# Performance work log

Measured on AMD Instinct MI355X. Metric: run time of the kernel, lower is better.

Reference implementation:

```python
import jax, jax.numpy as jnp
import numpy as np

EPS = 1e-6
H = 16       # query heads
KVH = 8      # kv heads
DH = 64      # head dim
HID = 1024


def _rms_norm(x, w, eps=EPS):
    ms = jnp.mean(jnp.square(x.astype(jnp.float32)), axis=-1, keepdims=True) + eps
    y = x.astype(jnp.float32) * jax.lax.rsqrt(ms)
    if w is not None:
        y = y * w.astype(jnp.float32)
    return y.astype(x.dtype)


def _rotate_half(x):
    h = x.shape[-1] // 2
    return jnp.concatenate([-x[..., h:], x[..., :h]], axis=-1)


def _multi_axis_rope(x, cos, sin, ndim):
    # x: [B,S,Hd,DH]; cos/sin: [S, rot_total]
    dh = x.shape[-1]
    rot = 2 * (dh // (2 * ndim))
    outs = []
    for i in range(ndim):
        sl = slice(i * rot, (i + 1) * rot)
        xp = x[..., sl]
        cp = cos[:, sl][:, None, :]   # [S,1,rot] broadcasts over heads
        sp = sin[:, sl][:, None, :]
        outs.append(xp * cp + _rotate_half(xp) * sp)
    return jnp.concatenate(outs, axis=-1)


def setup_inputs() -> dict:
    key = jax.random.key(0)
    ks = jax.random.split(key, 10)
    B, S = 4, 2048
    inp = {
        "hidden_states": jax.random.normal(ks[0], (B, S, HID), dtype=jnp.float32),
        "cos": jax.random.uniform(ks[1], (S, DH), dtype=jnp.float32, minval=-1.0, maxval=1.0),
        "sin": jax.random.uniform(ks[2], (S, DH), dtype=jnp.float32, minval=-1.0, maxval=1.0),
        "position_ids": jax.random.randint(ks[3], (B, S, 2), 0, 64).astype(jnp.int64),
        "attention_mask": jnp.ones((B, S), dtype=bool),
        "Wq": jax.random.normal(ks[4], (HID, H * DH), dtype=jnp.float32) * 0.02,
        "Wk": jax.random.normal(ks[5], (HID, KVH * DH), dtype=jnp.float32) * 0.02,
        "Wv": jax.random.normal(ks[6], (HID, KVH * DH), dtype=jnp.float32) * 0.02,
        "Wo": jax.random.normal(ks[7], (H * DH, HID), dtype=jnp.float32) * 0.02,
        "q_norm_w": jnp.ones((DH,), dtype=jnp.float32),
        "k_norm_w": jnp.ones((DH,), dtype=jnp.float32),
    }
    return inp


def reference(hidden_states, cos, sin, position_ids, attention_mask, Wq, Wk, Wv, Wo, q_norm_w, k_norm_w):
    B, S, _ = hidden_states.shape
    ndim = int(position_ids.shape[-1])

    q = (hidden_states @ Wq).reshape(B, S, H, DH)
    k = (hidden_states @ Wk).reshape(B, S, KVH, DH)
    v = (hidden_states @ Wv).reshape(B, S, KVH, DH)

    q = _rms_norm(q, q_norm_w)
    k = _rms_norm(k, k_norm_w)
    v = _rms_norm(v, None)  # v_norm has no scale

    q = _multi_axis_rope(q, cos, sin, ndim)
    k = _multi_axis_rope(k, cos, sin, ndim)

    # [B, heads, S, DH]; repeat kv heads for GQA
    q = q.transpose(0, 2, 1, 3)
    k = jnp.repeat(k.transpose(0, 2, 1, 3), H // KVH, axis=1)
    v = jnp.repeat(v.transpose(0, 2, 1, 3), H // KVH, axis=1)

    scores = jnp.einsum("bhqd,bhkd->bhqk", q, k)  # scaling = 1.0
    key_mask = attention_mask[:, None, None, :]
    scores = jnp.where(key_mask, scores, jnp.finfo(scores.dtype).min)
    probs = jax.nn.softmax(scores.astype(jnp.float32), axis=-1).astype(v.dtype)

    out = jnp.einsum("bhqk,bhkd->bhqd", probs, v)
    out = out.transpose(0, 2, 1, 3).reshape(B, S, H * DH)
    out = jnp.where(attention_mask[:, :, None], out, 0.0)
    return out @ Wo
```

## Files before the change

kernel.cpp:

```cpp
#include <hip/hip_runtime.h>
#include <stdint.h>
#include <stddef.h>

typedef unsigned short u16;
typedef unsigned int   u32;
typedef unsigned short u16x8 __attribute__((ext_vector_type(8)));
typedef unsigned int   u32x2 __attribute__((ext_vector_type(2)));
typedef __attribute__((ext_vector_type(8))) __bf16 bf16x8;
typedef __attribute__((ext_vector_type(4))) float f32x4;

__device__ __forceinline__ float bf2f(u16 v){
  union { unsigned u; float f; } x; x.u = ((unsigned)v) << 16; return x.f;
}
__device__ __forceinline__ u16 f2bf(float f){
  union { float f; unsigned u; } x; x.f = f;
  return (u16)((x.u + 0x7fffu + ((x.u >> 16) & 1u)) >> 16);
}

__device__ __forceinline__ float exp2_fast(float x){
  float r; asm("v_exp_f32 %0, %1" : "=v"(r) : "v"(x)); return r;
}
__device__ __forceinline__ u32 cvt_pk_bf16(float lo, float hi){
  u32 r; asm("v_cvt_pk_bf16_f32 %0, %1, %2" : "=v"(r) : "v"(lo), "v"(hi)); return r;
}

__device__ __forceinline__ f32x4 mfma16(bf16x8 a, bf16x8 b, f32x4 c){
  return __builtin_amdgcn_mfma_f32_16x16x32_bf16(a, b, c, 0, 0, 0);
}

#define AS1 __attribute__((address_space(1)))
#define AS3 __attribute__((address_space(3)))
__device__ __forceinline__ void gload_lds16(const void* g, void* l){
  __builtin_amdgcn_global_load_lds((const AS1 void*)g, (AS3 void*)l, 16, 0, 0);
}

__global__ void f32_to_bf16_swz(const float* __restrict__ in, u16* __restrict__ out,
                                int total_chunks){
  for (int i = blockIdx.x * blockDim.x + threadIdx.x; i < total_chunks;
       i += gridDim.x * blockDim.x){
    int row = i >> 7, c = i & 127;
    int cs = (c & ~7) | ((c & 7) ^ (row & 7));
    const float* p = in + ((size_t)i << 3);
    float4 v0 = *(const float4*)p;
    float4 v1 = *(const float4*)(p + 4);
    u16x8 o = { f2bf(v0.x), f2bf(v0.y), f2bf(v0.z), f2bf(v0.w),
                f2bf(v1.x), f2bf(v1.y), f2bf(v1.z), f2bf(v1.w) };
    *(u16x8*)(out + (((size_t)row << 7) + cs) * 8) = o;
  }
}

__global__ void conv_transpose_swz(const float* __restrict__ in, u16* __restrict__ out,
                                   int R, int C){
  __shared__ float t[32][33];
  int c0 = blockIdx.x * 32, r0 = blockIdx.y * 32;
  int tx = threadIdx.x, ty = threadIdx.y;
  t[ty][tx] = in[(size_t)(r0 + ty) * C + c0 + tx];
  __syncthreads();
  int tid = ty * 32 + tx;
  if (tid < 128){
    int orow = tid >> 2, oc = tid & 3;
    int gr = c0 + orow;
    int gc = (r0 >> 3) + oc;
    int gcs = (gc & ~7) | ((gc & 7) ^ (gr & 7));
    u16x8 v;
#pragma unroll
    for (int i = 0; i < 8; i++) v[i] = f2bf(t[oc * 8 + i][orow]);
    *(u16x8*)(out + (size_t)gr * R + gcs * 8) = v;
  }
}

__global__ void pack_cs(const float* __restrict__ cosb, const float* __restrict__ sinb,
                        float2* __restrict__ cs, int n){
  int i = blockIdx.x * 256 + threadIdx.x;
  if (i < n) cs[i] = (float2){cosb[i], sinb[i]};
}

template<int BM, int WM, int EPI>
__global__ __launch_bounds__(512, 2)
void gemm256(const u16* __restrict__ A, const u16* __restrict__ Bt,
             void* __restrict__ Cv, int M, int N, int K,
             const float2* __restrict__ cs, const float* __restrict__ qw,
             const float* __restrict__ kw, u16* __restrict__ Qn,
             u16* __restrict__ Kn, u16* __restrict__ Vn){
  constexpr int MF = WM / 16;
  constexpr int ALOADS = BM / 64;
  __shared__ __align__(16) u16 Ab[3][BM * 64];
  const int tid = threadIdx.x;
  const int wid = tid >> 6, lane = tid & 63;
  const int g = lane >> 4, col = lane & 15;
  const int wm = wid >> 2, wn = wid & 3;
  const int swz = col & 7;

  int nb  = gridDim.x * gridDim.y;
  int lid = blockIdx.y * gridDim.x + blockIdx.x;
  int cpx = nb >> 3;
  int sid = (lid & 7) * cpx + (lid >> 3);
  int bx  = sid % gridDim.x, by = sid / gridDim.x;
  const int m0 = by * BM, n0 = bx * 256;

  f32x4 acc[MF][4];
#pragma unroll
  for (int i = 0; i < MF; i++)
#pragma unroll
    for (int j = 0; j < 4; j++) acc[i][j] = (f32x4){0.f, 0.f, 0.f, 0.f};

  const int arow = wid * 8 + (lane >> 3);
  const int acl  = (lane & 7) * 8;

  auto STAGE_A = [&](int bi, int k0){
#pragma unroll
    for (int j = 0; j < ALOADS; j++)
      gload_lds16(A + (size_t)(m0 + j * 64 + arow) * K + k0 + acl,
                  &Ab[bi][j * 4096 + wid * 512]);
  };

  const int NT = K >> 6;
  STAGE_A(0, 0);
  STAGE_A(1, 64);
  if (ALOADS == 4) asm volatile("s_waitcnt vmcnt(4)");
  else             asm volatile("s_waitcnt vmcnt(2)");
  __builtin_amdgcn_sched_barrier(0);
  __builtin_amdgcn_s_barrier();
  __builtin_amdgcn_sched_barrier(0);

  int cb = 0, sa = 2;
  for (int t = 0; t < NT; ++t){
    bf16x8 bfr[4][2];
#pragma unroll
    for (int ni = 0; ni < 4; ni++){
      const u16* bp = Bt + (size_t)(n0 + wn * 64 + ni * 16 + col) * K + t * 64;
#pragma unroll
      for (int ks = 0; ks < 2; ks++)
        bfr[ni][ks] = *(const bf16x8*)(bp + (((ks * 4 + g) ^ swz) << 3));
    }
    __builtin_amdgcn_sched_barrier(0);
    if (t + 2 < NT) STAGE_A(sa, (t + 2) * 64);
    __builtin_amdgcn_sched_barrier(0);

    const u16* Ac = &Ab[cb][0];
#pragma unroll
    for (int ph = 0; ph < MF / 4; ++ph){
      bf16x8 afr[4][2];
#pragma unroll
      for (int m2 = 0; m2 < 4; m2++){
        int row = wm * WM + (ph * 4 + m2) * 16 + col;
#pragma unroll
        for (int ks = 0; ks < 2; ks++)
          afr[m2][ks] = *(const bf16x8*)&Ac[row * 64 + (((ks * 4 + g) ^ swz) << 3)];
      }
      __builtin_amdgcn_s_setprio(1);
#pragma unroll
      for (int m2 = 0; m2 < 4; m2++)
#pragma unroll
        for (int ni = 0; ni < 4; ni++)
#pragma unroll
          for (int ks = 0; ks < 2; ks++)
            acc[ph * 4 + m2][ni] =
                mfma16(afr[m2][ks], bfr[ni][ks], acc[ph * 4 + m2][ni]);
      __builtin_amdgcn_s_setprio(0);
    }

    asm volatile("s_waitcnt lgkmcnt(0)");
    __builtin_amdgcn_sched_barrier(0);
    if (t + 2 < NT){
      if (ALOADS == 4) asm volatile("s_waitcnt vmcnt(4)");
      else             asm volatile("s_waitcnt vmcnt(2)");
    } else {
      asm volatile("s_waitcnt vmcnt(0)");
    }
    __builtin_amdgcn_sched_barrier(0);
    __builtin_amdgcn_s_barrier();
    __builtin_amdgcn_sched_barrier(0);
    cb = (cb == 2) ? 0 : cb + 1;
    sa = (sa == 2) ? 0 : sa + 1;
  }

  if (EPI == 1){
    const int colbase = n0 + wn * 64;
    const int t0 = m0 + wm * WM;
    const int bb = t0 >> 11;
    if (colbase < 1536){
      const bool isQ = colbase < 1024;
      const int head = isQ ? (colbase >> 6) : ((colbase - 1024) >> 6);
      const float* wp = isQ ? qw : kw;
      float wv[4];
#pragma unroll
      for (int ni = 0; ni < 4; ni++) wv[ni] = wp[ni * 16 + col];
      u16* outp = isQ ? Qn : Kn;
      size_t hb = isQ ? ((size_t)(bb * 16 + head) * 2048)
                      : ((size_t)(bb * 8 + head) * 2048);
#pragma unroll
      for (int mi = 0; mi < MF; mi++){
        f32x4 ssv = (f32x4){0.f, 0.f, 0.f, 0.f};
#pragma unroll
        for (int ni = 0; ni < 4; ni++)
#pragma unroll
          for (int r = 0; r < 4; r++) ssv[r] += acc[mi][ni][r] * acc[mi][ni][r];
#pragma unroll
        for (int off = 1; off < 16; off <<= 1)
#pragma unroll
          for (int r = 0; r < 4; r++) ssv[r] += __shfl_xor(ssv[r], off, 64);
        f32x4 rinv;
#pragma unroll
        for (int r = 0; r < 4; r++) rinv[r] = rsqrtf(ssv[r] * (1.f / 64.f) + 1e-6f);
        int s0 = (t0 + mi * 16 + g * 4) & 2047;
#pragma unroll
        for (int np = 0; np < 2; np++){
          int d0 = np * 32 + col, d1 = d0 + 16;
#pragma unroll
          for (int r = 0; r < 4; r++){
            int s = s0 + r;
            float y0 = acc[mi][np * 2][r]     * rinv[r] * wv[np * 2];
            float y1 = acc[mi][np * 2 + 1][r] * rinv[r] * wv[np * 2 + 1];
            float2 c0 = cs[s * 64 + d0];
            float2 c1 = cs[s * 64 + d1];
            float o0 = y0 * c0.x - y1 * c0.y;
            float o1 = y1 * c1.x + y0 * c1.y;
            if (isQ){
              outp[(hb + s) * 64 + d0] = f2bf(o0);
              outp[(hb + s) * 64 + d1] = f2bf(o1);
            } else {
              int z0 = ((((d0 >> 3) ^ s) & 7) << 3) | (d0 & 7);
              int z1 = ((((d1 >> 3) ^ s) & 7) << 3) | (d1 & 7);
              outp[(hb + s) * 64 + z0] = f2bf(o0);
              outp[(hb + s) * 64 + z1] = f2bf(o1);
            }
          }
        }
      }
    } else {
      const int kvh = (colbase - 1536) >> 6;
      const size_t vb0 = (size_t)(bb * 8 + kvh) * 64;
#pragma unroll
      for (int mi = 0; mi < MF; mi++){
        f32x4 ssv = (f32x4){0.f, 0.f, 0.f, 0.f};
#pragma unroll
        for (int ni = 0; ni < 4; ni++)
#pragma unroll
          for (int r = 0; r < 4; r++) ssv[r] += acc[mi][ni][r] * acc[mi][ni][r];
#pragma unroll
        for (int off = 1; off < 16; off <<= 1)
#pragma unroll
          for (int r = 0; r < 4; r++) ssv[r] += __shfl_xor(ssv[r], off, 64);
        f32x4 rinv;
#pragma unroll
        for (int r = 0; r < 4; r++) rinv[r] = rsqrtf(ssv[r] * (1.f / 64.f) + 1e-6f);
        int s0 = (t0 + mi * 16 + g * 4) & 2047;
#pragma unroll
        for (int ni = 0; ni < 4; ni++){
          int d = ni * 16 + col;
          uint2 o;
          o.x = cvt_pk_bf16(acc[mi][ni][0] * rinv[0], acc[mi][ni][1] * rinv[1]);
          o.y = cvt_pk_bf16(acc[mi][ni][2] * rinv[2], acc[mi][ni][3] * rinv[3]);
          size_t addr = (vb0 + d) * 2048 + (s0 & ~63)
                      + ((((s0 >> 3) ^ (d & 7)) & 7) << 3) + (s0 & 7);
          *(uint2*)(Vn + addr) = o;
        }
      }
    }
    return;
  }

#pragma unroll
  for (int mi = 0; mi < MF; mi++)
#pragma unroll
    for (int ni = 0; ni < 4; ni++)
#pragma unroll
      for (int r = 0; r < 4; r++){
        int row = m0 + wm * WM + mi * 16 + g * 4 + r;
        int cc  = n0 + wn * 64 + ni * 16 + col;
        ((float*)Cv)[(size_t)row * N + cc] = acc[mi][ni][r];
      }
}

__global__ __launch_bounds__(512, 2)
void flash_attn(const u16* __restrict__ Qn, const u16* __restrict__ Kn,
                const u16* __restrict__ Vn, u16* __restrict__ AO){
  const int S = 2048;
  const float L2E = 1.4426950408889634f;
  const float C2 = 30.f;
  const int i = blockIdx.x;
  const int hb = (i & 7) | ((i >> 6) << 3);
  const int qt = (i >> 3) & 7;
  const int h = hb & 15, b = hb >> 4;
  const int kvh = h >> 1;
  const int wid = threadIdx.x >> 6, lane = threadIdx.x & 63;
  const int kg = wid >> 2, wq = wid & 3;
  const int g = lane >> 4, col = lane & 15;
  const int q0 = qt * 256 + wq * 64;

  __shared__ __align__(16) u16 lds[34816];
  u16* Kl = lds + kg * 8192;
  u16* Vl = lds + 16384 + kg * 8192;

  bf16x8 ones;
#pragma unroll
  for (int k = 0; k < 8; k++) ones[k] = (__bf16)1.0f;

  bf16x8 aq[4][2];
#pragma unroll
  for (int cg = 0; cg < 4; cg++){
    const u16* qp = Qn + ((size_t)((b * 16 + h) * S) + q0 + cg * 16 + col) * 64;
    aq[cg][0] = *(const bf16x8*)(qp + g * 8);
    aq[cg][1] = *(const bf16x8*)(qp + 32 + g * 8);
  }

  const u16* Kbase = Kn + (size_t)(b * 8 + kvh) * S * 64 + (size_t)kg * 1024 * 64;
  const u16* Vbase = Vn + (size_t)(b * 8 + kvh) * 64 * S;
  const int vcol0 = kg * 1024;

  f32x4 acc[4][4];
  f32x4 lacc[4];
#pragma unroll
  for (int cg = 0; cg < 4; cg++){
    lacc[cg] = (f32x4){0.f, 0.f, 0.f, 0.f};
#pragma unroll
    for (int k = 0; k < 4; k++) acc[cg][k] = (f32x4){0.f, 0.f, 0.f, 0.f};
  }

  const int sw = col & 7;

  auto STAGE = [&](int bi, int ktl){
    int kc0 = ktl * 64;
#pragma unroll
    for (int cc = 0; cc < 2; cc++){
      int chunk = cc * 4 + wq;
      gload_lds16(Kbase + (size_t)kc0 * 64 + chunk * 512 + lane * 8,
                  Kl + bi * 4096 + chunk * 512);
      int drow = chunk * 8 + (lane >> 3);
      gload_lds16(Vbase + (size_t)drow * S + vcol0 + kc0 + (lane & 7) * 8,
                  Vl + bi * 4096 + chunk * 512);
    }
  };

  int buf = 0;
  STAGE(0, 0);
  __syncthreads();

  for (int kt = 0; kt < 16; ++kt){
    if (kt + 1 < 16) STAGE(buf ^ 1, kt + 1);

    const u16* Kb = Kl + buf * 4096;
    const u16* Vb = Vl + buf * 4096;

    bf16x8 kf[4][2], vf[4][2];
#pragma unroll
    for (int c = 0; c < 4; c++){
      const u16* kb = Kb + (c * 16 + col) * 64;
      kf[c][0] = *(const bf16x8*)(kb + (g ^ sw) * 8);
      kf[c][1] = *(const bf16x8*)(kb + ((4 + g) ^ sw) * 8);
      const u16* vb = Vb + (c * 16 + col) * 64;
      vf[c][0] = *(const bf16x8*)(vb + (g ^ sw) * 8);
      vf[c][1] = *(const bf16x8*)(vb + ((4 + g) ^ sw) * 8);
    }

#pragma unroll
    for (int cg = 0; cg < 4; cg++){
      f32x4 sf[4];
      __builtin_amdgcn_s_setprio(1);
#pragma unroll
      for (int c = 0; c < 4; c++){
        f32x4 z = (f32x4){0.f, 0.f, 0.f, 0.f};
        z = mfma16(kf[c][0], aq[cg][0], z);
        sf[c] = mfma16(kf[c][1], aq[cg][1], z);
      }
      __builtin_amdgcn_s_setprio(0);

      uint2 pw[4];
#pragma unroll
      for (int c = 0; c < 4; c++){
        float p0 = exp2_fast(__builtin_fmaf(sf[c][0], L2E, -C2));
        float p1 = exp2_fast(__builtin_fmaf(sf[c][1], L2E, -C2));
        float p2 = exp2_fast(__builtin_fmaf(sf[c][2], L2E, -C2));
        float p3 = exp2_fast(__builtin_fmaf(sf[c][3], L2E, -C2));
        pw[c].x = cvt_pk_bf16(p0, p1);
        pw[c].y = cvt_pk_bf16(p2, p3);
      }

      bf16x8 pf[2];
#pragma unroll
      for (int sp = 0; sp < 2; sp++){
        u32x2 tx = __builtin_amdgcn_permlane32_swap(pw[sp*2].x, pw[sp*2+1].x, false, false);
        u32x2 fx = __builtin_amdgcn_permlane16_swap(tx.x, tx.y, false, false);
        u32x2 ty = __builtin_amdgcn_permlane32_swap(pw[sp*2].y, pw[sp*2+1].y, false, false);
        u32x2 fy = __builtin_amdgcn_permlane16_swap(ty.x, ty.y, false, false);
        union { u32 w[4]; bf16x8 v; } pu;
        pu.w[0] = fx.x;
        pu.w[1] = fy.x;
        pu.w[2] = fx.y;
        pu.w[3] = fy.y;
        pf[sp] = pu.v;
      }

      __builtin_amdgcn_s_setprio(1);
#pragma unroll
      for (int cd = 0; cd < 4; cd++){
        acc[cg][cd] = mfma16(vf[cd][0], pf[0], acc[cg][cd]);
        acc[cg][cd] = mfma16(vf[cd][1], pf[1], acc[cg][cd]);
      }
      lacc[cg] = mfma16(ones, pf[0], lacc[cg]);
      lacc[cg] = mfma16(ones, pf[1], lacc[cg]);
      __builtin_amdgcn_s_setprio(0);
    }

    __syncthreads();
    buf ^= 1;
  }

  f32x4* sAcc = (f32x4*)lds;
  float*  sL  = (float*)((char*)lds + 65536);
  if (kg == 1){
#pragma unroll
    for (int cg = 0; cg < 4; cg++){
#pragma unroll
      for (int cd = 0; cd < 4; cd++)
        sAcc[(cg * 4 + cd) * 256 + wq * 64 + lane] = acc[cg][cd];
      sL[cg * 256 + wq * 64 + lane] = lacc[cg][0];
    }
  }
  __syncthreads();
  if (kg == 0){
#pragma unroll
    for (int cg = 0; cg < 4; cg++){
      float l = lacc[cg][0] + sL[cg * 256 + wq * 64 + lane];
      float linv = 1.f / l;
      int s = q0 + cg * 16 + col;
#pragma unroll
      for (int cd = 0; cd < 4; cd++){
        f32x4 a = acc[cg][cd] + sAcc[(cg * 4 + cd) * 256 + wq * 64 + lane];
        uint2 o;
        o.x = cvt_pk_bf16(a[0] * linv, a[1] * linv);
        o.y = cvt_pk_bf16(a[2] * linv, a[3] * linv);
        int pc = (cd * 2 + (g >> 1)) ^ sw;
        *(uint2*)(AO + (size_t)(b * S + s) * 1024 + h * 64 + pc * 8 + (g & 1) * 4) = o;
      }
    }
  }
}

extern "C" void kernel_launch(void* const* d_in, const int* in_sizes, int n_in,
                              void* d_out, int out_size, void* d_ws, size_t ws_size,
                              hipStream_t stream){
  const int Btok = 8192;
  const float* hs   = (const float*)d_in[0];
  const float* cosb = (const float*)d_in[1];
  const float* sinb = (const float*)d_in[2];
  const float* Wq = (const float*)d_in[5];
  const float* Wk = (const float*)d_in[6];
  const float* Wv = (const float*)d_in[7];
  const float* Wo = (const float*)d_in[8];
  const float* qw = (const float*)d_in[9];
  const float* kw = (const float*)d_in[10];
  float* out = (float*)d_out;

  char* ws = (char*)d_ws;
  u16* hsB   = (u16*)ws;               ws += (size_t)Btok * 1024 * 2;
  u16* WqkvT = (u16*)ws;               ws += (size_t)2048 * 1024 * 2;
  u16* WoT   = (u16*)ws;               ws += (size_t)1024 * 1024 * 2;
  u16* Qn    = (u16*)ws;               ws += (size_t)Btok * 1024 * 2;
  u16* Kn    = (u16*)ws;               ws += (size_t)Btok * 512  * 2;
  u16* Vn    = (u16*)ws;               ws += (size_t)Btok * 512  * 2;
  float2* cst = (float2*)ws;           ws += (size_t)2048 * 64 * 8;
  u16* AO    = hsB;

  f32_to_bf16_swz<<<2048, 256, 0, stream>>>(hs, hsB, Btok * 128);

  dim3 tb(32, 32);
  conv_transpose_swz<<<dim3(32, 32), tb, 0, stream>>>(Wq, WqkvT,               1024, 1024);
  conv_transpose_swz<<<dim3(16, 32), tb, 0, stream>>>(Wk, WqkvT + 1024 * 1024, 1024, 512);
  conv_transpose_swz<<<dim3(16, 32), tb, 0, stream>>>(Wv, WqkvT + 1536 * 1024, 1024, 512);
  conv_transpose_swz<<<dim3(32, 32), tb, 0, stream>>>(Wo, WoT,                 1024, 1024);
  pack_cs<<<512, 256, 0, stream>>>(cosb, sinb, cst, 2048 * 64);

  gemm256<256, 128, 1><<<dim3(8, 32), 512, 0, stream>>>(
      hsB, WqkvT, nullptr, Btok, 2048, 1024, cst, qw, kw, Qn, Kn, Vn);

  flash_attn<<<512, 512, 0, stream>>>(Qn, Kn, Vn, AO);

  gemm256<128, 64, 2><<<dim3(4, 64), 512, 0, stream>>>(
      AO, WoT, out, Btok, 1024, 1024, nullptr, nullptr, nullptr,
      nullptr, nullptr, nullptr);
}
```

Measured before the change: 184.2 us.

## Stage B tiles through LDS with double buffering and merge prep kernels

The GEMM now loads both A and B tiles into LDS with async global-to-LDS copies, double-buffered, instead of triple-buffering only A and reading B fragments directly from global memory. The six conversion and transpose launches are combined into one prep kernel dispatched by block index, to cut launch overhead. LDS use per block grows considerably, which may lower occupancy. The pipeline depth shrinks to one tile in flight, with a full vmcnt wait each iteration.

Result: faster. 173.3 us (-5.9%).

```diff
diff --git a/kernel.cpp b/kernel.cpp
--- a/kernel.cpp
+++ b/kernel.cpp
@@ -34,57 +34,63 @@
   __builtin_amdgcn_global_load_lds((const AS1 void*)g, (AS3 void*)l, 16, 0, 0);
 }
 
-__global__ void f32_to_bf16_swz(const float* __restrict__ in, u16* __restrict__ out,
-                                int total_chunks){
-  for (int i = blockIdx.x * blockDim.x + threadIdx.x; i < total_chunks;
-       i += gridDim.x * blockDim.x){
-    int row = i >> 7, c = i & 127;
-    int cs = (c & ~7) | ((c & 7) ^ (row & 7));
-    const float* p = in + ((size_t)i << 3);
-    float4 v0 = *(const float4*)p;
-    float4 v1 = *(const float4*)(p + 4);
-    u16x8 o = { f2bf(v0.x), f2bf(v0.y), f2bf(v0.z), f2bf(v0.w),
-                f2bf(v1.x), f2bf(v1.y), f2bf(v1.z), f2bf(v1.w) };
-    *(u16x8*)(out + (((size_t)row << 7) + cs) * 8) = o;
-  }
-}
-
-__global__ void conv_transpose_swz(const float* __restrict__ in, u16* __restrict__ out,
-                                   int R, int C){
-  __shared__ float t[32][33];
-  int c0 = blockIdx.x * 32, r0 = blockIdx.y * 32;
-  int tx = threadIdx.x, ty = threadIdx.y;
-  t[ty][tx] = in[(size_t)(r0 + ty) * C + c0 + tx];
-  __syncthreads();
-  int tid = ty * 32 + tx;
-  if (tid < 128){
-    int orow = tid >> 2, oc = tid & 3;
-    int gr = c0 + orow;
-    int gc = (r0 >> 3) + oc;
-    int gcs = (gc & ~7) | ((gc & 7) ^ (gr & 7));
-    u16x8 v;
-#pragma unroll
-    for (int i = 0; i < 8; i++) v[i] = f2bf(t[oc * 8 + i][orow]);
-    *(u16x8*)(out + (size_t)gr * R + gcs * 8) = v;
-  }
-}
-
-__global__ void pack_cs(const float* __restrict__ cosb, const float* __restrict__ sinb,
-                        float2* __restrict__ cs, int n){
-  int i = blockIdx.x * 256 + threadIdx.x;
-  if (i < n) cs[i] = (float2){cosb[i], sinb[i]};
+__global__ void prep_all(const float* __restrict__ hs, u16* __restrict__ hsB,
+                         const float* __restrict__ Wq, const float* __restrict__ Wk,
+                         const float* __restrict__ Wv, const float* __restrict__ Wo,
+                         u16* __restrict__ WqkvT, u16* __restrict__ WoT,
+                         const float* __restrict__ cosb, const float* __restrict__ sinb,
+                         float2* __restrict__ cs){
+  __shared__ float tbuf[32][33];
+  const int blk = blockIdx.x;
+  const int t = threadIdx.x;
+  if (blk < 3072){
+    const float* in; u16* out; int C, bx, by;
+    if (blk < 1024){ in = Wq; out = WqkvT; C = 1024; bx = blk & 31; by = blk >> 5; }
+    else if (blk < 1536){ int q = blk - 1024; in = Wk; out = WqkvT + 1024 * 1024; C = 512; bx = q & 15; by = q >> 4; }
+    else if (blk < 2048){ int q = blk - 1536; in = Wv; out = WqkvT + 1536 * 1024; C = 512; bx = q & 15; by = q >> 4; }
+    else { int q = blk - 2048; in = Wo; out = WoT; C = 1024; bx = q & 31; by = q >> 5; }
+    int tx = t & 31, ty = t >> 5;
+    int c0 = bx * 32, r0 = by * 32;
+    tbuf[ty][tx] = in[(size_t)(r0 + ty) * C + c0 + tx];
+    __syncthreads();
+    if (t < 128){
+      int orow = t >> 2, oc = t & 3;
+      int gr = c0 + orow;
+      int gc = (r0 >> 3) + oc;
+      int gcs = (gc & ~7) | ((gc & 7) ^ (gr & 7));
+      u16x8 v;
+#pragma unroll
+      for (int i = 0; i < 8; i++) v[i] = f2bf(tbuf[oc * 8 + i][orow]);
+      *(u16x8*)(out + (size_t)gr * 1024 + gcs * 8) = v;
+    }
+  } else if (blk < 3584){
+    for (int i = (blk - 3072) * 1024 + t; i < 1048576; i += 524288){
+      int row = i >> 7, c = i & 127;
+      int cst = (c & ~7) | ((c & 7) ^ (row & 7));
+      const float* p = hs + ((size_t)i << 3);
+      float4 v0 = *(const float4*)p;
+      float4 v1 = *(const float4*)(p + 4);
+      u16x8 o = { f2bf(v0.x), f2bf(v0.y), f2bf(v0.z), f2bf(v0.w),
+                  f2bf(v1.x), f2bf(v1.y), f2bf(v1.z), f2bf(v1.w) };
+      *(u16x8*)(hsB + (((size_t)row << 7) + cst) * 8) = o;
+    }
+  } else {
+    int i = (blk - 3584) * 1024 + t;
+    cs[i] = (float2){cosb[i], sinb[i]};
+  }
 }
 
 template<int BM, int WM, int EPI>
 __global__ __launch_bounds__(512, 2)
-void gemm256(const u16* __restrict__ A, const u16* __restrict__ Bt,
-             void* __restrict__ Cv, int M, int N, int K,
-             const float2* __restrict__ cs, const float* __restrict__ qw,
-             const float* __restrict__ kw, u16* __restrict__ Qn,
-             u16* __restrict__ Kn, u16* __restrict__ Vn){
+void gemmB(const u16* __restrict__ A, const u16* __restrict__ Bt,
+           void* __restrict__ Cv, int M, int N, int K,
+           const float2* __restrict__ cs, const float* __restrict__ qw,
+           const float* __restrict__ kw, u16* __restrict__ Qn,
+           u16* __restrict__ Kn, u16* __restrict__ Vn){
   constexpr int MF = WM / 16;
   constexpr int ALOADS = BM / 64;
-  __shared__ __align__(16) u16 Ab[3][BM * 64];
+  __shared__ __align__(16) u16 Ab[2][BM * 64];
+  __shared__ __align__(16) u16 Bb[2][256 * 64];
   const int tid = threadIdx.x;
   const int wid = tid >> 6, lane = tid & 63;
   const int g = lane >> 4, col = lane & 15;
@@ -107,37 +113,39 @@
   const int arow = wid * 8 + (lane >> 3);
   const int acl  = (lane & 7) * 8;
 
-  auto STAGE_A = [&](int bi, int k0){
+  auto STAGE = [&](int bi, int k0){
 #pragma unroll
     for (int j = 0; j < ALOADS; j++)
       gload_lds16(A + (size_t)(m0 + j * 64 + arow) * K + k0 + acl,
                   &Ab[bi][j * 4096 + wid * 512]);
+#pragma unroll
+    for (int j = 0; j < 4; j++)
+      gload_lds16(Bt + (size_t)(n0 + j * 64 + arow) * K + k0 + acl,
+                  &Bb[bi][j * 4096 + wid * 512]);
   };
 
   const int NT = K >> 6;
-  STAGE_A(0, 0);
-  STAGE_A(1, 64);
-  if (ALOADS == 4) asm volatile("s_waitcnt vmcnt(4)");
-  else             asm volatile("s_waitcnt vmcnt(2)");
+  STAGE(0, 0);
+  asm volatile("s_waitcnt vmcnt(0)");
   __builtin_amdgcn_sched_barrier(0);
   __builtin_amdgcn_s_barrier();
   __builtin_amdgcn_sched_barrier(0);
 
-  int cb = 0, sa = 2;
+  int buf = 0;
   for (int t = 0; t < NT; ++t){
+    if (t + 1 < NT) STAGE(buf ^ 1, (t + 1) * 64);
+    __builtin_amdgcn_sched_barrier(0);
+
+    const u16* Ac = &Ab[buf][0];
+    const u16* Bc = &Bb[buf][0];
     bf16x8 bfr[4][2];
 #pragma unroll
     for (int ni = 0; ni < 4; ni++){
-      const u16* bp = Bt + (size_t)(n0 + wn * 64 + ni * 16 + col) * K + t * 64;
+      int row = wn * 64 + ni * 16 + col;
 #pragma unroll
       for (int ks = 0; ks < 2; ks++)
-        bfr[ni][ks] = *(const bf16x8*)(bp + (((ks * 4 + g) ^ swz) << 3));
-    }
-    __builtin_amdgcn_sched_barrier(0);
-    if (t + 2 < NT) STAGE_A(sa, (t + 2) * 64);
-    __builtin_amdgcn_sched_barrier(0);
-
-    const u16* Ac = &Ab[cb][0];
+        bfr[ni][ks] = *(const bf16x8*)&Bc[row * 64 + (((ks * 4 + g) ^ swz) << 3)];
+    }
 #pragma unroll
     for (int ph = 0; ph < MF / 4; ++ph){
       bf16x8 afr[4][2];
@@ -162,17 +170,11 @@
 
     asm volatile("s_waitcnt lgkmcnt(0)");
     __builtin_amdgcn_sched_barrier(0);
-    if (t + 2 < NT){
-      if (ALOADS == 4) asm volatile("s_waitcnt vmcnt(4)");
-      else             asm volatile("s_waitcnt vmcnt(2)");
-    } else {
-      asm volatile("s_waitcnt vmcnt(0)");
-    }
+    asm volatile("s_waitcnt vmcnt(0)");
     __builtin_amdgcn_sched_barrier(0);
     __builtin_amdgcn_s_barrier();
     __builtin_amdgcn_sched_barrier(0);
-    cb = (cb == 2) ? 0 : cb + 1;
-    sa = (sa == 2) ? 0 : sa + 1;
+    buf ^= 1;
   }
 
   if (EPI == 1){
@@ -463,21 +465,15 @@
   float2* cst = (float2*)ws;           ws += (size_t)2048 * 64 * 8;
   u16* AO    = hsB;
 
-  f32_to_bf16_swz<<<2048, 256, 0, stream>>>(hs, hsB, Btok * 128);
-
-  dim3 tb(32, 32);
-  conv_transpose_swz<<<dim3(32, 32), tb, 0, stream>>>(Wq, WqkvT,               1024, 1024);
-  conv_transpose_swz<<<dim3(16, 32), tb, 0, stream>>>(Wk, WqkvT + 1024 * 1024, 1024, 512);
-  conv_transpose_swz<<<dim3(16, 32), tb, 0, stream>>>(Wv, WqkvT + 1536 * 1024, 1024, 512);
-  conv_transpose_swz<<<dim3(32, 32), tb, 0, stream>>>(Wo, WoT,                 1024, 1024);
-  pack_cs<<<512, 256, 0, stream>>>(cosb, sinb, cst, 2048 * 64);
-
-  gemm256<256, 128, 1><<<dim3(8, 32), 512, 0, stream>>>(
+  prep_all<<<3712, 1024, 0, stream>>>(hs, hsB, Wq, Wk, Wv, Wo, WqkvT, WoT,
+                                      cosb, sinb, cst);
+
+  gemmB<256, 128, 1><<<dim3(8, 32), 512, 0, stream>>>(
       hsB, WqkvT, nullptr, Btok, 2048, 1024, cst, qw, kw, Qn, Kn, Vn);
 
   flash_attn<<<512, 512, 0, stream>>>(Qn, Kn, Vn, AO);
 
-  gemm256<128, 64, 2><<<dim3(4, 64), 512, 0, stream>>>(
+  gemmB<128, 64, 2><<<dim3(4, 64), 512, 0, stream>>>(
       AO, WoT, out, Btok, 1024, 1024, nullptr, nullptr, nullptr,
       nullptr, nullptr, nullptr);
 }
```
